# Kernel tuning notes

Measured on AMD Instinct MI355X. Metric: run time of the kernel, lower is better.

## Reference

```python
import jax, jax.numpy as jnp
import numpy as np

L, E, H, NH, S_MAX, V, NL = 3, 512, 64, 8, 512, 30522, 2  # layers, d_model, head_dim, heads, max_len, vocab, labels
LN_EPS = 1e-5


def _layer_norm(x, g, b):
    m = jnp.mean(x, axis=-1, keepdims=True)
    v = jnp.mean((x - m) ** 2, axis=-1, keepdims=True)
    return (x - m) * jax.lax.rsqrt(v + LN_EPS) * g + b


def setup_inputs() -> dict:
    key = jax.random.key(0)
    ks = jax.random.split(key, 20)
    B, S = 32, 512
    inp = {
        'input_ids': jax.random.randint(ks[0], (B, S), 0, V, dtype=jnp.int64 if jax.config.jax_enable_x64 else jnp.int32),
        'attention_mask': jnp.ones((B, S), dtype=jnp.int32),
        # embeddings (padding_idx=0 row zeroed, as in nn.Embedding(padding_idx=0))
        'emb': (0.02 * jax.random.normal(ks[1], (V, E), jnp.float32)).at[0].set(0.0),
        'pos_emb': 0.02 * jax.random.normal(ks[2], (S_MAX, E), jnp.float32),
        # per-layer stacked params, leading dim = L
        'in_proj_w': 0.02 * jax.random.normal(ks[3], (L, 3 * E, E), jnp.float32),
        'in_proj_b': jnp.zeros((L, 3 * E), jnp.float32),
        'out_proj_w': 0.02 * jax.random.normal(ks[4], (L, E, E), jnp.float32),
        'out_proj_b': jnp.zeros((L, E), jnp.float32),
        'ln1_g': jnp.ones((L, E), jnp.float32), 'ln1_b': jnp.zeros((L, E), jnp.float32),
        'ln2_g': jnp.ones((L, E), jnp.float32), 'ln2_b': jnp.zeros((L, E), jnp.float32),
        'ffn1_w': 0.02 * jax.random.normal(ks[5], (L, 4 * E, E), jnp.float32),
        'ffn1_b': jnp.zeros((L, 4 * E), jnp.float32),
        'ffn2_w': 0.02 * jax.random.normal(ks[6], (L, E, 4 * E), jnp.float32),
        'ffn2_b': jnp.zeros((L, E), jnp.float32),
        'cls_w': 0.02 * jax.random.normal(ks[7], (NL, E), jnp.float32),
        'cls_b': jnp.zeros((NL,), jnp.float32),
    }
    return inp


def reference(input_ids, attention_mask, emb, pos_emb, in_proj_w, in_proj_b,
              out_proj_w, out_proj_b, ln1_g, ln1_b, ln2_g, ln2_b,
              ffn1_w, ffn1_b, ffn2_w, ffn2_b, cls_w, cls_b):
    B, S = input_ids.shape
    x = emb[input_ids] + pos_emb[jnp.arange(S)][None, :, :]  # [B,S,E]
    # key_padding_mask: True where attention_mask == 0 -> -inf on key axis
    kpm_bias = jnp.where((attention_mask == 0)[:, None, None, :], -jnp.inf, 0.0)  # [B,1,1,S]
    scale = 1.0 / np.sqrt(H)
    attns = []
    for l in range(L):
        qkv = x @ in_proj_w[l].T + in_proj_b[l]          # [B,S,3E]
        q, k, v = jnp.split(qkv, 3, axis=-1)
        q = q.reshape(B, S, NH, H).transpose(0, 2, 1, 3)  # [B,NH,S,H]
        k = k.reshape(B, S, NH, H).transpose(0, 2, 1, 3)
        v = v.reshape(B, S, NH, H).transpose(0, 2, 1, 3)
        scores = jnp.einsum('bhqd,bhkd->bhqk', q, k) * scale + kpm_bias
        a = jax.nn.softmax(scores, axis=-1)               # materialized per-head weights [B,NH,S,S]
        o = jnp.einsum('bhqk,bhkd->bhqd', a, v).transpose(0, 2, 1, 3).reshape(B, S, E)
        o = o @ out_proj_w[l].T + out_proj_b[l]
        x = _layer_norm(x + o, ln1_g[l], ln1_b[l])
        f = jax.nn.gelu(x @ ffn1_w[l].T + ffn1_b[l], approximate=False)
        f = f @ ffn2_w[l].T + ffn2_b[l]
        x = _layer_norm(x + f, ln2_g[l], ln2_b[l])
        attns.append(a)
    logits = x[:, 0, :] @ cls_w.T + cls_b                 # CLS token head
    return logits, jnp.stack(attns)                       # ([B,NL], [L,B,NH,S,S])
```

## Files before the change

kernel.cpp:

```cpp
#include <hip/hip_runtime.h>
#include <hip/hip_bf16.h>


typedef __bf16 bf16_t;
typedef __bf16 bf16x4 __attribute__((ext_vector_type(4)));
typedef __bf16 bf16x8 __attribute__((ext_vector_type(8)));
typedef float  f32x4  __attribute__((ext_vector_type(4)));

__device__ __forceinline__ void gld16(const bf16_t* g, bf16_t* l) {
    __builtin_amdgcn_global_load_lds((const __attribute__((address_space(1))) void*)g,
                                     (__attribute__((address_space(3))) void*)l, 16, 0, 0);
}

__global__ __launch_bounds__(256) void cvt_bf16(
    const float* __restrict__ s, bf16_t* __restrict__ d)
{
    int g = blockIdx.x * 256 + threadIdx.x;
    float4 v = ((const float4*)s)[g];
    bf16x4 p;
    p[0] = (bf16_t)v.x; p[1] = (bf16_t)v.y; p[2] = (bf16_t)v.z; p[3] = (bf16_t)v.w;
    ((bf16x4*)d)[g] = p;
}

__global__ __launch_bounds__(256) void embed_kernel(
    const int* __restrict__ ids, const float* __restrict__ emb,
    const float* __restrict__ pos, float* __restrict__ x, bf16_t* __restrict__ xb)
{
    int g = blockIdx.x * 256 + threadIdx.x;
    int token = g >> 7, c4 = g & 127;
    int id = ids[token];
    float4 e = ((const float4*)emb)[(long long)id * 128 + c4];
    float4 p = ((const float4*)pos)[(long long)(token & 511) * 128 + c4];
    e.x += p.x; e.y += p.y; e.z += p.z; e.w += p.w;
    ((float4*)x)[g] = e;
    bf16x4 h;
    h[0] = (bf16_t)e.x; h[1] = (bf16_t)e.y; h[2] = (bf16_t)e.z; h[3] = (bf16_t)e.w;
    ((bf16x4*)xb)[g] = h;
}

template<int BN, int AF32, int GELU, int OBF>
__global__ __launch_bounds__(256) void gemm_m97(
    const void* __restrict__ Ap, const bf16_t* __restrict__ Bp,
    void* __restrict__ Cp, const float* __restrict__ bias,
    int lda, int ldb, int ldc, int K,
    long long sAb, long long sAh, long long sBb, long long sBh,
    long long sCb, long long sCh, float alpha)
{
    constexpr int WR = (BN == 128) ? 2 : 4;
    constexpr int WM = 128 / WR;
    constexpr int MI = WM / 16;

    __shared__ __align__(16) bf16_t As[128 * 64];
    __shared__ __align__(16) bf16_t Bs[BN * 64];

    const int m0 = blockIdx.x * 128, n0 = blockIdx.y * BN;
    const int z = blockIdx.z, zb = z >> 3, zh = z & 7;

    const bf16_t* A  = (const bf16_t*)Ap;
    const float*  Af = (const float*)Ap;
    if (AF32) Af += zb * sAb + zh * sAh + (long long)m0 * lda;
    else      A  += zb * sAb + zh * sAh + (long long)m0 * lda;
    const bf16_t* B = Bp + zb * sBb + zh * sBh + (long long)n0 * ldb;

    const int tid = threadIdx.x, wave = tid >> 6, lane = tid & 63;
    const int q = lane >> 4, r = lane & 15;
    const int wr = wave % WR, wc = wave / WR;

    f32x4 acc[MI][4];
#pragma unroll
    for (int i = 0; i < MI; i++)
#pragma unroll
        for (int j = 0; j < 4; j++) acc[i][j] = (f32x4){0.f, 0.f, 0.f, 0.f};

    for (int k0 = 0; k0 < K; k0 += 64) {
        if (AF32) {
#pragma unroll
            for (int it = 0; it < 8; it++) {
                int chunk = it * 256 + tid;
                int row = chunk >> 4, c4 = (chunk & 15) << 2;
                float4 v = *(const float4*)(Af + (long long)row * lda + k0 + c4);
                bf16x4 p;
                p[0] = (bf16_t)v.x; p[1] = (bf16_t)v.y; p[2] = (bf16_t)v.z; p[3] = (bf16_t)v.w;
                *(bf16x4*)(As + row * 64 + c4) = p;
            }
        } else {
#pragma unroll
            for (int it = 0; it < 4; it++) {
                int chunk = it * 256 + tid;
                int row = chunk >> 3, c8 = (chunk & 7) << 3;
                gld16(A + (long long)row * lda + k0 + c8,
                      As + (it * 256 + wave * 64) * 8);
            }
        }
#pragma unroll
        for (int it = 0; it < BN / 32; it++) {
            int chunk = it * 256 + tid;
            int row = chunk >> 3, c8 = (chunk & 7) << 3;
            gld16(B + (long long)row * ldb + k0 + c8,
                  Bs + (it * 256 + wave * 64) * 8);
        }
        __syncthreads();
#pragma unroll
        for (int kk = 0; kk < 64; kk += 32) {
            bf16x8 av[MI], bv[4];
#pragma unroll
            for (int mi = 0; mi < MI; mi++)
                av[mi] = *(const bf16x8*)(As + (wr * WM + mi * 16 + r) * 64 + kk + q * 8);
#pragma unroll
            for (int ni = 0; ni < 4; ni++)
                bv[ni] = *(const bf16x8*)(Bs + (wc * 64 + ni * 16 + r) * 64 + kk + q * 8);
#pragma unroll
            for (int mi = 0; mi < MI; mi++)
#pragma unroll
                for (int ni = 0; ni < 4; ni++)
                    acc[mi][ni] = __builtin_amdgcn_mfma_f32_16x16x32_bf16(
                        av[mi], bv[ni], acc[mi][ni], 0, 0, 0);
        }
        __syncthreads();
    }

    const long long cb = (long long)zb * sCb + (long long)zh * sCh;
#pragma unroll
    for (int ni = 0; ni < 4; ni++) {
        int col = n0 + wc * 64 + ni * 16 + r;
        float bvl = bias ? bias[col] : 0.f;
#pragma unroll
        for (int mi = 0; mi < MI; mi++) {
#pragma unroll
            for (int i = 0; i < 4; i++) {
                int row = m0 + wr * WM + mi * 16 + q * 4 + i;
                float v = acc[mi][ni][i] * alpha + bvl;
                if (GELU) v = 0.5f * v * (1.f + erff(v * 0.70710678118654752f));
                if (OBF) ((bf16_t*)Cp)[cb + (long long)row * ldc + col] = (bf16_t)v;
                else     ((float*)Cp)[cb + (long long)row * ldc + col] = v;
            }
        }
    }
}

__global__ __launch_bounds__(256) void transpose_v(
    const bf16_t* __restrict__ qkv, bf16_t* __restrict__ Vt)
{
    int z = blockIdx.x, b = z >> 3, h = z & 7;
    int k0 = blockIdx.y * 64;
    __shared__ bf16_t t[64][72];
    const bf16_t* src = qkv + (long long)(b * 512 + k0) * 1536 + 1024 + h * 64;
    int tid = threadIdx.x;
#pragma unroll
    for (int it = 0; it < 2; it++) {
        int idx = tid + 256 * it;
        int i = idx >> 3, j8 = (idx & 7) << 3;
        bf16x8 v = *(const bf16x8*)(src + (long long)i * 1536 + j8);
#pragma unroll
        for (int j = 0; j < 8; j++) t[i][j8 + j] = v[j];
    }
    __syncthreads();
    bf16_t* dst = Vt + (long long)z * 32768 + k0;
#pragma unroll
    for (int it = 0; it < 2; it++) {
        int idx = tid + 256 * it;
        int d = idx >> 3, kx = (idx & 7) << 3;
        bf16x8 v;
#pragma unroll
        for (int j = 0; j < 8; j++) v[j] = t[kx + j][d];
        *(bf16x8*)(dst + (long long)d * 512 + kx) = v;
    }
}

__global__ __launch_bounds__(256) void softmax_kernel(
    float* __restrict__ a, const int* __restrict__ amask)
{
    long long row = (long long)blockIdx.x * 4 + (threadIdx.x >> 6);
    int lane = threadIdx.x & 63;
    int b = (int)(row >> 12);
    float* p = a + row * 512;
    const int* mrow = amask + b * 512;

    float v[8];
    float mx = -3.0e38f;
#pragma unroll
    for (int i = 0; i < 2; i++) {
        float4 t = ((const float4*)p)[lane + 64 * i];
        int k0 = (lane + 64 * i) * 4;
        float tv[4] = {t.x, t.y, t.z, t.w};
#pragma unroll
        for (int c = 0; c < 4; c++) {
            float s = (mrow[k0 + c] == 0) ? -__builtin_inff() : tv[c];
            v[i * 4 + c] = s;
            mx = fmaxf(mx, s);
        }
    }
#pragma unroll
    for (int o = 32; o; o >>= 1) mx = fmaxf(mx, __shfl_xor(mx, o));
    float sum = 0.f;
#pragma unroll
    for (int j = 0; j < 8; j++) { v[j] = __expf(v[j] - mx); sum += v[j]; }
#pragma unroll
    for (int o = 32; o; o >>= 1) sum += __shfl_xor(sum, o);
    float inv = 1.f / sum;
#pragma unroll
    for (int i = 0; i < 2; i++) {
        float4 t;
        t.x = v[i * 4 + 0] * inv; t.y = v[i * 4 + 1] * inv;
        t.z = v[i * 4 + 2] * inv; t.w = v[i * 4 + 3] * inv;
        ((float4*)p)[lane + 64 * i] = t;
    }
}

__global__ __launch_bounds__(256) void add_ln(
    float* __restrict__ x, const float* __restrict__ rsd,
    const float* __restrict__ g, const float* __restrict__ bta,
    bf16_t* __restrict__ xb)
{
    long long row = (long long)blockIdx.x * 4 + (threadIdx.x >> 6);
    int lane = threadIdx.x & 63;
    float4* xr = (float4*)(x + row * 512);
    const float4* rr = (const float4*)(rsd + row * 512);
    float4 s0 = xr[lane], s1 = xr[lane + 64];
    float4 r0 = rr[lane], r1 = rr[lane + 64];
    s0.x += r0.x; s0.y += r0.y; s0.z += r0.z; s0.w += r0.w;
    s1.x += r1.x; s1.y += r1.y; s1.z += r1.z; s1.w += r1.w;
    float sum = s0.x + s0.y + s0.z + s0.w + s1.x + s1.y + s1.z + s1.w;
    float sq  = s0.x*s0.x + s0.y*s0.y + s0.z*s0.z + s0.w*s0.w
              + s1.x*s1.x + s1.y*s1.y + s1.z*s1.z + s1.w*s1.w;
#pragma unroll
    for (int o = 32; o; o >>= 1) { sum += __shfl_xor(sum, o); sq += __shfl_xor(sq, o); }
    float mean = sum * (1.f / 512.f);
    float var  = sq * (1.f / 512.f) - mean * mean;
    float rstd = rsqrtf(var + 1e-5f);
    const float4* g4 = (const float4*)g;
    const float4* b4 = (const float4*)bta;
    float4 gg = g4[lane], bb = b4[lane], o0;
    o0.x = (s0.x - mean) * rstd * gg.x + bb.x;
    o0.y = (s0.y - mean) * rstd * gg.y + bb.y;
    o0.z = (s0.z - mean) * rstd * gg.z + bb.z;
    o0.w = (s0.w - mean) * rstd * gg.w + bb.w;
    xr[lane] = o0;
    bf16x4 h0;
    h0[0] = (bf16_t)o0.x; h0[1] = (bf16_t)o0.y; h0[2] = (bf16_t)o0.z; h0[3] = (bf16_t)o0.w;
    *(bf16x4*)(xb + row * 512 + lane * 4) = h0;
    gg = g4[lane + 64]; bb = b4[lane + 64];
    float4 o1;
    o1.x = (s1.x - mean) * rstd * gg.x + bb.x;
    o1.y = (s1.y - mean) * rstd * gg.y + bb.y;
    o1.z = (s1.z - mean) * rstd * gg.z + bb.z;
    o1.w = (s1.w - mean) * rstd * gg.w + bb.w;
    xr[lane + 64] = o1;
    bf16x4 h1;
    h1[0] = (bf16_t)o1.x; h1[1] = (bf16_t)o1.y; h1[2] = (bf16_t)o1.z; h1[3] = (bf16_t)o1.w;
    *(bf16x4*)(xb + row * 512 + 256 + lane * 4) = h1;
}

__global__ void cls_head(const float* __restrict__ x, const float* __restrict__ w,
                         const float* __restrict__ cb, float* __restrict__ out)
{
    int b = blockIdx.x >> 1, c = blockIdx.x & 1;
    int lane = threadIdx.x;
    const float* xr = x + (long long)b * 512 * 512;
    const float* wr = w + c * 512;
    float s = 0.f;
#pragma unroll
    for (int i = 0; i < 8; i++) s += xr[lane + 64 * i] * wr[lane + 64 * i];
#pragma unroll
    for (int o = 32; o; o >>= 1) s += __shfl_xor(s, o);
    if (lane == 0) out[b * 2 + c] = s + cb[c];
}

extern "C" void kernel_launch(void* const* d_in, const int* in_sizes, int n_in,
                              void* d_out, int out_size, void* d_ws, size_t ws_size,
                              hipStream_t stream)
{
    const int*   ids   = (const int*)d_in[0];
    const int*   amask = (const int*)d_in[1];
    const float* emb   = (const float*)d_in[2];
    const float* pos   = (const float*)d_in[3];
    const float* in_w  = (const float*)d_in[4];
    const float* in_b  = (const float*)d_in[5];
    const float* out_w = (const float*)d_in[6];
    const float* out_b = (const float*)d_in[7];
    const float* ln1g  = (const float*)d_in[8];
    const float* ln1b  = (const float*)d_in[9];
    const float* ln2g  = (const float*)d_in[10];
    const float* ln2b  = (const float*)d_in[11];
    const float* f1w   = (const float*)d_in[12];
    const float* f1b   = (const float*)d_in[13];
    const float* f2w   = (const float*)d_in[14];
    const float* f2b   = (const float*)d_in[15];
    const float* clsw  = (const float*)d_in[16];
    const float* clsb  = (const float*)d_in[17];

    float* outp = (float*)d_out;
    float* ws = (float*)d_ws;
    float*  x    = ws;
    bf16_t* xb   = (bf16_t*)(ws + 8388608);
    float*  pg   = ws + 12582912;
    bf16_t* Ob   = (bf16_t*)(ws + 20971520);
    bf16_t* qkvb = (bf16_t*)(ws + 25165824);
    bf16_t* Vt   = (bf16_t*)(ws + 37748736);
    bf16_t* fb   = qkvb;
    bf16_t* wb   = (bf16_t*)(ws + 41943040);
    bf16_t* w_in  = wb;
    bf16_t* w_out = wb + 2359296;
    bf16_t* w_f1  = wb + 3145728;
    bf16_t* w_f2  = wb + 6291456;

    cvt_bf16<<<2304, 256, 0, stream>>>(in_w,  w_in);
    cvt_bf16<<< 768, 256, 0, stream>>>(out_w, w_out);
    cvt_bf16<<<3072, 256, 0, stream>>>(f1w,   w_f1);
    cvt_bf16<<<3072, 256, 0, stream>>>(f2w,   w_f2);

    embed_kernel<<<8192, 256, 0, stream>>>(ids, emb, pos, x, xb);

    for (int l = 0; l < 3; l++) {
        float* attnL = outp + 64 + (long long)l * 67108864;

        gemm_m97<128, 0, 0, 1><<<dim3(128, 12, 1), 256, 0, stream>>>(
            xb, w_in + (long long)l * 786432, qkvb, in_b + l * 1536,
            512, 512, 1536, 512, 0, 0, 0, 0, 0, 0, 1.f);

        transpose_v<<<dim3(256, 8), 256, 0, stream>>>(qkvb, Vt);

        gemm_m97<128, 0, 0, 0><<<dim3(4, 4, 256), 256, 0, stream>>>(
            qkvb, qkvb + 512, attnL, nullptr,
            1536, 1536, 512, 64,
            786432, 64, 786432, 64, 2097152, 262144, 0.125f);

        softmax_kernel<<<32768, 256, 0, stream>>>(attnL, amask);

        gemm_m97<64, 1, 0, 1><<<dim3(4, 1, 256), 256, 0, stream>>>(
            attnL, Vt, Ob, nullptr,
            512, 512, 512, 512,
            2097152, 262144, 262144, 32768, 262144, 64, 1.f);

        gemm_m97<128, 0, 0, 0><<<dim3(128, 4, 1), 256, 0, stream>>>(
            Ob, w_out + (long long)l * 262144, pg, out_b + l * 512,
            512, 512, 512, 512, 0, 0, 0, 0, 0, 0, 1.f);

        add_ln<<<4096, 256, 0, stream>>>(x, pg, ln1g + l * 512, ln1b + l * 512, xb);

        gemm_m97<128, 0, 1, 1><<<dim3(128, 16, 1), 256, 0, stream>>>(
            xb, w_f1 + (long long)l * 1048576, fb, f1b + l * 2048,
            512, 512, 2048, 512, 0, 0, 0, 0, 0, 0, 1.f);

        gemm_m97<128, 0, 0, 0><<<dim3(128, 4, 1), 256, 0, stream>>>(
            fb, w_f2 + (long long)l * 1048576, pg, f2b + l * 512,
            2048, 2048, 512, 2048, 0, 0, 0, 0, 0, 0, 1.f);

        add_ln<<<4096, 256, 0, stream>>>(x, pg, ln2g + l * 512, ln2b + l * 512, xb);
    }

    cls_head<<<64, 64, 0, stream>>>(x, clsw, clsb, outp);
}
```

Measured before the change: 2.205 ms.

## Fuse QK^T scores GEMM with masked softmax into one attention kernel

Replaces the separate batched scores GEMM and row softmax kernels with one kernel per (batch, head, 64-query block). The kernel stages all 512 keys in LDS, computes scores with MFMA, and applies the scale, mask, max, exp and normalisation in registers before writing the fp32 probabilities once. This removes a full write and read-back of the 256 MB attention tensor per layer. In exchange it uses 128 accumulator registers per thread and 66 KB of LDS, which limits occupancy, and its output stores are strided scalar writes.

After: 2.069 ms. 6.2% less time.

```diff
diff --git a/kernel.cpp b/kernel.cpp
--- a/kernel.cpp
+++ b/kernel.cpp
@@ -138,6 +138,89 @@
     }
 }
 
+__global__ __launch_bounds__(256) void attn_scores_softmax(
+    const bf16_t* __restrict__ qkv, const int* __restrict__ amask,
+    float* __restrict__ attn)
+{
+    __shared__ __align__(16) bf16_t Ks[512 * 64];
+    __shared__ float bias_s[512];
+
+    const int z = blockIdx.y, b = z >> 3, h = z & 7;
+    const int q0 = blockIdx.x * 64;
+    const int tid = threadIdx.x, wave = tid >> 6, lane = tid & 63;
+    const int q = lane >> 4, r = lane & 15;
+
+    const bf16_t* Kg = qkv + (long long)(b * 512) * 1536 + 512 + h * 64;
+#pragma unroll
+    for (int it = 0; it < 16; it++) {
+        int chunk = it * 256 + tid;
+        int row = chunk >> 3, c8 = (chunk & 7) << 3;
+        gld16(Kg + (long long)row * 1536 + c8, Ks + (it * 256 + wave * 64) * 8);
+    }
+    {
+        int i0 = tid * 2;
+        bias_s[i0]     = (amask[b * 512 + i0]     == 0) ? -__builtin_inff() : 0.f;
+        bias_s[i0 + 1] = (amask[b * 512 + i0 + 1] == 0) ? -__builtin_inff() : 0.f;
+    }
+    const bf16_t* Qg = qkv + (long long)(b * 512 + q0 + wave * 16 + r) * 1536 + h * 64;
+    bf16x8 av0 = *(const bf16x8*)(Qg + q * 8);
+    bf16x8 av1 = *(const bf16x8*)(Qg + 32 + q * 8);
+    __syncthreads();
+
+    f32x4 acc[32];
+#pragma unroll
+    for (int nf = 0; nf < 32; nf++) acc[nf] = (f32x4){0.f, 0.f, 0.f, 0.f};
+
+#pragma unroll
+    for (int nf = 0; nf < 32; nf++) {
+        bf16x8 b0 = *(const bf16x8*)(Ks + (nf * 16 + r) * 64 + q * 8);
+        bf16x8 b1 = *(const bf16x8*)(Ks + (nf * 16 + r) * 64 + 32 + q * 8);
+        acc[nf] = __builtin_amdgcn_mfma_f32_16x16x32_bf16(av0, b0, acc[nf], 0, 0, 0);
+        acc[nf] = __builtin_amdgcn_mfma_f32_16x16x32_bf16(av1, b1, acc[nf], 0, 0, 0);
+    }
+
+    float mx[4] = {-3.0e38f, -3.0e38f, -3.0e38f, -3.0e38f};
+#pragma unroll
+    for (int nf = 0; nf < 32; nf++) {
+        float bl = bias_s[nf * 16 + r];
+#pragma unroll
+        for (int i = 0; i < 4; i++) {
+            float s = acc[nf][i] * 0.125f + bl;
+            acc[nf][i] = s;
+            mx[i] = fmaxf(mx[i], s);
+        }
+    }
+#pragma unroll
+    for (int off = 8; off; off >>= 1)
+#pragma unroll
+        for (int i = 0; i < 4; i++) mx[i] = fmaxf(mx[i], __shfl_xor(mx[i], off));
+
+    float sm[4] = {0.f, 0.f, 0.f, 0.f};
+#pragma unroll
+    for (int nf = 0; nf < 32; nf++)
+#pragma unroll
+        for (int i = 0; i < 4; i++) {
+            float e = __expf(acc[nf][i] - mx[i]);
+            acc[nf][i] = e;
+            sm[i] += e;
+        }
+#pragma unroll
+    for (int off = 8; off; off >>= 1)
+#pragma unroll
+        for (int i = 0; i < 4; i++) sm[i] += __shfl_xor(sm[i], off);
+
+    float inv[4];
+#pragma unroll
+    for (int i = 0; i < 4; i++) inv[i] = 1.f / sm[i];
+
+    float* out = attn + (long long)z * 262144 + (long long)(q0 + wave * 16) * 512;
+#pragma unroll
+    for (int nf = 0; nf < 32; nf++)
+#pragma unroll
+        for (int i = 0; i < 4; i++)
+            out[(q * 4 + i) * 512 + nf * 16 + r] = acc[nf][i] * inv[i];
+}
+
 __global__ __launch_bounds__(256) void transpose_v(
     const bf16_t* __restrict__ qkv, bf16_t* __restrict__ Vt)
 {
@@ -164,46 +247,6 @@
 #pragma unroll
         for (int j = 0; j < 8; j++) v[j] = t[kx + j][d];
         *(bf16x8*)(dst + (long long)d * 512 + kx) = v;
-    }
-}
-
-__global__ __launch_bounds__(256) void softmax_kernel(
-    float* __restrict__ a, const int* __restrict__ amask)
-{
-    long long row = (long long)blockIdx.x * 4 + (threadIdx.x >> 6);
-    int lane = threadIdx.x & 63;
-    int b = (int)(row >> 12);
-    float* p = a + row * 512;
-    const int* mrow = amask + b * 512;
-
-    float v[8];
-    float mx = -3.0e38f;
-#pragma unroll
-    for (int i = 0; i < 2; i++) {
-        float4 t = ((const float4*)p)[lane + 64 * i];
-        int k0 = (lane + 64 * i) * 4;
-        float tv[4] = {t.x, t.y, t.z, t.w};
-#pragma unroll
-        for (int c = 0; c < 4; c++) {
-            float s = (mrow[k0 + c] == 0) ? -__builtin_inff() : tv[c];
-            v[i * 4 + c] = s;
-            mx = fmaxf(mx, s);
-        }
-    }
-#pragma unroll
-    for (int o = 32; o; o >>= 1) mx = fmaxf(mx, __shfl_xor(mx, o));
-    float sum = 0.f;
-#pragma unroll
-    for (int j = 0; j < 8; j++) { v[j] = __expf(v[j] - mx); sum += v[j]; }
-#pragma unroll
-    for (int o = 32; o; o >>= 1) sum += __shfl_xor(sum, o);
-    float inv = 1.f / sum;
-#pragma unroll
-    for (int i = 0; i < 2; i++) {
-        float4 t;
-        t.x = v[i * 4 + 0] * inv; t.y = v[i * 4 + 1] * inv;
-        t.z = v[i * 4 + 2] * inv; t.w = v[i * 4 + 3] * inv;
-        ((float4*)p)[lane + 64 * i] = t;
     }
 }
 
@@ -320,12 +363,7 @@
 
         transpose_v<<<dim3(256, 8), 256, 0, stream>>>(qkvb, Vt);
 
-        gemm_m97<128, 0, 0, 0><<<dim3(4, 4, 256), 256, 0, stream>>>(
-            qkvb, qkvb + 512, attnL, nullptr,
-            1536, 1536, 512, 64,
-            786432, 64, 786432, 64, 2097152, 262144, 0.125f);
-
-        softmax_kernel<<<32768, 256, 0, stream>>>(attnL, amask);
+        attn_scores_softmax<<<dim3(8, 256), 256, 0, stream>>>(qkvb, amask, attnL);
 
         gemm_m97<64, 1, 0, 1><<<dim3(4, 1, 256), 256, 0, stream>>>(
             attnL, Vt, Ob, nullptr,
```
